# Performance work log

Hardware: AMD Instinct MI355X
Metric: run time of the kernel (lower is better)

## Reference

```python
import jax, jax.numpy as jnp
import numpy as np


def _maxpool2(x):
    # 2x2 max pool, stride 2, valid padding (H, W even). x: [B,H,W,C]
    B, H, W, C = x.shape
    return x.reshape(B, H // 2, 2, W // 2, 2, C).max(axis=(2, 4))


def setup_inputs() -> dict:
    key = jax.random.key(0)
    ks = jax.random.split(key, 9)
    B, H, W, C = 8, 64, 64, 512
    cfg, ch = C // 8, C // 2
    std = 0.02
    return {
        "x": jax.random.normal(ks[0], (B, H, W, C), jnp.float32),
        "theta_w": jax.random.normal(ks[1], (C, cfg), jnp.float32) * std,
        "theta_b": jnp.zeros((cfg,), jnp.float32),
        "phi_w": jax.random.normal(ks[2], (C, cfg), jnp.float32) * std,
        "phi_b": jnp.zeros((cfg,), jnp.float32),
        "g_w": jax.random.normal(ks[3], (C, ch), jnp.float32) * std,
        "g_b": jnp.zeros((ch,), jnp.float32),
        "o3_w": jax.random.normal(ks[4], (ch, C), jnp.float32) * std,
        "o3_b": jnp.zeros((C,), jnp.float32),
        # original initializes gamma to 0; use 0.1 so the attention branch contributes
        "gamma": jnp.full((1,), 0.1, jnp.float32),
    }


def reference(x, theta_w, theta_b, phi_w, phi_b, g_w, g_b, o3_w, o3_b, gamma):
    B, H, W, C = x.shape
    cfg = theta_w.shape[1]
    ch = g_w.shape[1]
    hw = H * W
    hwd = (H // 2) * (W // 2)

    theta = jnp.einsum("bhwc,cf->bhwf", x, theta_w) + theta_b          # [B,H,W,cfg]
    phi = _maxpool2(jnp.einsum("bhwc,cf->bhwf", x, phi_w) + phi_b)     # [B,H/2,W/2,cfg]
    g = _maxpool2(jnp.einsum("bhwc,cg->bhwg", x, g_w) + g_b)           # [B,H/2,W/2,ch]

    theta_f = theta.reshape(B, hw, cfg)
    phi_f = phi.reshape(B, hwd, cfg)
    g_f = g.reshape(B, hwd, ch)

    # s[b,i,j] = phi[b,i] . theta[b,j]; softmax over j (last axis, Keras default)
    s = jnp.einsum("bif,bjf->bij", phi_f, theta_f)                     # [B,hwd,hw]
    beta = jax.nn.softmax(s, axis=-1)
    # o = matmul(beta, g, transpose_a=True): o[b,j,c] = sum_i beta[b,i,j] g[b,i,c]
    o = jnp.einsum("bij,bic->bjc", beta, g_f)                          # [B,hw,ch]
    o = o.reshape(B, H, W, ch)
    o = jnp.einsum("bhwg,gc->bhwc", o, o3_w) + o3_b                    # [B,H,W,C]
    return gamma * o + x
```

## Files before the change

kernel.cpp:

```cpp
#include <hip/hip_runtime.h>
#include <cstdint>

typedef short short8 __attribute__((ext_vector_type(8)));
typedef float floatx4 __attribute__((ext_vector_type(4)));

__device__ __forceinline__ unsigned short f2bf(float f) {
    unsigned int u = __builtin_bit_cast(unsigned int, f);
    u += 0x7FFFu + ((u >> 16) & 1u);
    return (unsigned short)(u >> 16);
}
__device__ __forceinline__ float bf2f(unsigned short h) {
    unsigned int u = ((unsigned int)h) << 16;
    return __builtin_bit_cast(float, u);
}

__device__ __forceinline__ void async_copy16(const void* g, void* lds) {
    __builtin_amdgcn_global_load_lds(
        (const __attribute__((address_space(1))) void*)g,
        (__attribute__((address_space(3))) void*)lds, 16, 0, 0);
}

__device__ __forceinline__ int swz(int row, int koff) {
    return koff ^ (((row >> 2) & 3) << 4);
}

template<bool AFP32, int EPI>
__global__ __launch_bounds__(256) void mfma_gemm(
    const void* __restrict__ Avoid, const unsigned short* __restrict__ B,
    void* __restrict__ Cout, const float* __restrict__ bias,
    const float* __restrict__ gamma, const float* __restrict__ resid,
    int lda, int ldb, int ldc, int K)
{
    __shared__ unsigned short As[4096];
    __shared__ unsigned short Bs[4096];

    const int tid = threadIdx.x;
    const int wv = tid >> 6, ln = tid & 63;
    const int r16 = ln & 15, q8 = ln >> 4;
    const int wm = (wv >> 1) * 64, wn = (wv & 1) * 64;
    const int m0 = blockIdx.x * 128, n0 = blockIdx.y * 128;

    floatx4 acc[4][4] = {};

    for (int k0 = 0; k0 < K; k0 += 32) {
        if (AFP32) {
            const float* Af = (const float*)Avoid;
            #pragma unroll
            for (int p = 0; p < 4; ++p) {
                int u = p * 256 + tid;
                int row = u >> 3, c4 = u & 7;
                float4 v = *(const float4*)(Af + (size_t)(m0 + row) * lda + k0 + c4 * 4);
                ushort4 h;
                h.x = f2bf(v.x); h.y = f2bf(v.y); h.z = f2bf(v.z); h.w = f2bf(v.w);
                *(ushort4*)&As[row * 32 + c4 * 4] = h;
            }
            #pragma unroll
            for (int q = 0; q < 2; ++q) {
                int chunk = wv * 2 + q;
                int e = (chunk << 9) + ln * 8;
                int row = e >> 5, col = e & 31;
                async_copy16(B + (size_t)(n0 + row) * ldb + (k0 + col), &Bs[chunk << 9]);
            }
        } else {
            const unsigned short* Ag = (const unsigned short*)Avoid;
            #pragma unroll
            for (int q = 0; q < 2; ++q) {
                int chunk = wv * 2 + q;
                int e = (chunk << 9) + ln * 8;
                int row = e >> 5, col = e & 31;
                async_copy16(Ag + (size_t)(m0 + row) * lda + (k0 + col), &As[chunk << 9]);
                async_copy16(B + (size_t)(n0 + row) * ldb + (k0 + col), &Bs[chunk << 9]);
            }
        }
        __syncthreads();

        short8 af[4], bff[4];
        #pragma unroll
        for (int i = 0; i < 4; ++i) {
            af[i]  = *(const short8*)&As[(wm + i * 16 + r16) * 32 + q8 * 8];
            bff[i] = *(const short8*)&Bs[(wn + i * 16 + r16) * 32 + q8 * 8];
        }
        #pragma unroll
        for (int mi = 0; mi < 4; ++mi)
            #pragma unroll
            for (int ni = 0; ni < 4; ++ni)
                acc[mi][ni] = __builtin_amdgcn_mfma_f32_16x16x32_bf16(
                    af[mi], bff[ni], acc[mi][ni], 0, 0, 0);
        __syncthreads();
    }

    if (EPI == 2) {
        float* C = (float*)Cout;
        const float gm = gamma[0];
        #pragma unroll
        for (int ni = 0; ni < 4; ++ni) {
            const int n = n0 + wn + ni * 16 + r16;
            const float bs = bias[n];
            #pragma unroll
            for (int mi = 0; mi < 4; ++mi)
                #pragma unroll
                for (int r = 0; r < 4; ++r) {
                    int m = m0 + wm + mi * 16 + q8 * 4 + r;
                    C[(size_t)m * ldc + n] = gm * (acc[mi][ni][r] + bs) + resid[(size_t)m * ldc + n];
                }
        }
    } else {
        unsigned short* C = (unsigned short*)Cout;
        #pragma unroll
        for (int ni = 0; ni < 4; ++ni) {
            const int n = n0 + wn + ni * 16 + r16;
            const float bs = bias[n];
            #pragma unroll
            for (int mi = 0; mi < 4; ++mi)
                #pragma unroll
                for (int r = 0; r < 4; ++r) {
                    int m = m0 + wm + mi * 16 + q8 * 4 + r;
                    C[(size_t)m * ldc + n] = f2bf(acc[mi][ni][r] + bs);
                }
        }
    }
}

__global__ __launch_bounds__(256) void phase1_l_kernel(
    const unsigned short* __restrict__ tpgF,
    const unsigned short* __restrict__ phiP,
    float* __restrict__ lbuf)
{
    __shared__ unsigned short th_s[8192];
    __shared__ unsigned short ph_s[4096];
    const int tid = threadIdx.x, wv = tid >> 6, ln = tid & 63;
    const int r16 = ln & 15, q8 = ln >> 4, lsub = ln >> 3, l8 = ln & 7;
    const int jsp = blockIdx.x, i0 = blockIdx.y * 64, b = blockIdx.z;

    #pragma unroll
    for (int q = 0; q < 2; ++q) {
        int chunk = wv * 2 + q, row = chunk * 8 + lsub;
        int so = swz(row, l8 * 8);
        async_copy16(phiP + (size_t)(b * 1024 + i0 + row) * 64 + so, &ph_s[chunk * 512]);
    }

    float colsum[4] = {0.f, 0.f, 0.f, 0.f};
    for (int jc = 0; jc < 8; ++jc) {
        const int j0 = jsp * 1024 + jc * 128;
        __syncthreads();
        #pragma unroll
        for (int q = 0; q < 4; ++q) {
            int chunk = wv * 4 + q, row = chunk * 8 + lsub;
            int so = swz(row, l8 * 8);
            async_copy16(tpgF + (size_t)(b * 4096 + j0 + row) * 384 + so, &th_s[chunk * 512]);
        }
        __syncthreads();

        floatx4 sacc[2][4] = {};
        #pragma unroll
        for (int ks = 0; ks < 2; ++ks) {
            short8 af[2], bf[4];
            #pragma unroll
            for (int mi = 0; mi < 2; ++mi)
                af[mi] = *(const short8*)&th_s[(wv * 32 + mi * 16 + r16) * 64 + swz(r16, ks * 32 + q8 * 8)];
            #pragma unroll
            for (int ni = 0; ni < 4; ++ni)
                bf[ni] = *(const short8*)&ph_s[(ni * 16 + r16) * 64 + swz(r16, ks * 32 + q8 * 8)];
            #pragma unroll
            for (int mi = 0; mi < 2; ++mi)
                #pragma unroll
                for (int ni = 0; ni < 4; ++ni)
                    sacc[mi][ni] = __builtin_amdgcn_mfma_f32_16x16x32_bf16(
                        af[mi], bf[ni], sacc[mi][ni], 0, 0, 0);
        }
        #pragma unroll
        for (int mi = 0; mi < 2; ++mi)
            #pragma unroll
            for (int ni = 0; ni < 4; ++ni)
                #pragma unroll
                for (int r = 0; r < 4; ++r)
                    colsum[ni] += __expf(sacc[mi][ni][r] - 20.f);
    }
    #pragma unroll
    for (int ni = 0; ni < 4; ++ni) {
        float s = colsum[ni];
        s += __shfl_xor(s, 16);
        s += __shfl_xor(s, 32);
        if (q8 == 0) atomicAdd(&lbuf[b * 1024 + i0 + ni * 16 + r16], s);
    }
}

__global__ __launch_bounds__(512) void attn_fused_kernel(
    const unsigned short* __restrict__ tpgF,
    const unsigned short* __restrict__ phiP,
    const unsigned short* __restrict__ gPT,
    unsigned short* __restrict__ o_)
{
    __shared__ unsigned short es0[8192];
    __shared__ unsigned short es1[8192];
    __shared__ unsigned short ph_s[4][4096];
    __shared__ unsigned short gs[2][16384];

    const int tid = threadIdx.x, wv = tid >> 6, ln = tid & 63;
    const int r16 = ln & 15, q8 = ln >> 4, lsub = ln >> 3, l8 = ln & 7;
    const int j0 = blockIdx.x * 128, b = blockIdx.y;
    const int jh = wv >> 2, it = wv & 3;

    #pragma unroll
    for (int q = 0; q < 2; ++q) {
        int chunk = wv * 2 + q, row = chunk * 8 + lsub;
        async_copy16(tpgF + (size_t)(b * 4096 + j0 + row) * 384 + swz(row, l8 * 8),
                     &es1[chunk * 512]);
    }
    {
        int prow = wv * 8 + lsub;
        async_copy16(phiP + (size_t)(b * 1024 + prow) * 64 + swz(prow, l8 * 8),
                     &ph_s[0][wv * 512]);
        #pragma unroll
        for (int q = 0; q < 4; ++q) {
            int chunk = wv * 4 + q, c = chunk * 8 + lsub;
            async_copy16(gPT + (size_t)(b * 256 + c) * 1024 + swz(c, l8 * 8),
                         &gs[0][chunk * 512]);
        }
        async_copy16(phiP + (size_t)(b * 1024 + 64 + prow) * 64 + swz(prow, l8 * 8),
                     &ph_s[1][wv * 512]);
    }
    asm volatile("s_waitcnt vmcnt(5)" ::: "memory");
    __builtin_amdgcn_sched_barrier(0);
    __builtin_amdgcn_s_barrier();
    __builtin_amdgcn_sched_barrier(0);

    short8 thf[4][2];
    #pragma unroll
    for (int mi = 0; mi < 4; ++mi)
        #pragma unroll
        for (int ks = 0; ks < 2; ++ks)
            thf[mi][ks] = *(const short8*)&es1[(jh * 64 + mi * 16 + r16) * 64
                                               + swz(r16, ks * 32 + q8 * 8)];

    {
        floatx4 sacc[4] = {};
        #pragma unroll
        for (int ks = 0; ks < 2; ++ks) {
            short8 pf = *(const short8*)&ph_s[0][(it * 16 + r16) * 64
                                                 + swz(r16, ks * 32 + q8 * 8)];
            #pragma unroll
            for (int mi = 0; mi < 4; ++mi)
                sacc[mi] = __builtin_amdgcn_mfma_f32_16x16x32_bf16(
                    thf[mi][ks], pf, sacc[mi], 0, 0, 0);
        }
        #pragma unroll
        for (int mi = 0; mi < 4; ++mi)
            #pragma unroll
            for (int r = 0; r < 4; ++r) {
                int j = jh * 64 + mi * 16 + q8 * 4 + r;
                es0[j * 64 + (((it ^ q8) << 4) | r16)] = f2bf(__expf(sacc[mi][r] - 20.f));
            }
    }
    asm volatile("s_waitcnt vmcnt(0) lgkmcnt(0)" ::: "memory");
    __builtin_amdgcn_sched_barrier(0);
    __builtin_amdgcn_s_barrier();
    __builtin_amdgcn_sched_barrier(0);

    floatx4 acc[4][4] = {};

    for (int t = 0; t < 16; ++t) {
        const int buf = t & 1, nbuf = buf ^ 1;
        unsigned short* esr = buf ? es1 : es0;
        unsigned short* esw = buf ? es0 : es1;
        const unsigned short* gsr = gs[buf];
        unsigned short* gsw = gs[nbuf];

        if (t < 15) {
            #pragma unroll
            for (int q = 0; q < 4; ++q) {
                int chunk = wv * 4 + q, c = chunk * 8 + lsub;
                async_copy16(gPT + (size_t)(b * 256 + c) * 1024 + (t + 1) * 64 + swz(c, l8 * 8),
                             &gsw[chunk * 512]);
            }
        }
        if (t < 14) {
            int prow = wv * 8 + lsub;
            async_copy16(phiP + (size_t)(b * 1024 + (t + 2) * 64 + prow) * 64 + swz(prow, l8 * 8),
                         &ph_s[(t + 2) & 3][wv * 512]);
        }

        if (t < 15) {
            const unsigned short* php = ph_s[(t + 1) & 3];
            floatx4 sacc[4] = {};
            #pragma unroll
            for (int ks = 0; ks < 2; ++ks) {
                short8 pf = *(const short8*)&php[(it * 16 + r16) * 64
                                                 + swz(r16, ks * 32 + q8 * 8)];
                #pragma unroll
                for (int mi = 0; mi < 4; ++mi)
                    sacc[mi] = __builtin_amdgcn_mfma_f32_16x16x32_bf16(
                        thf[mi][ks], pf, sacc[mi], 0, 0, 0);
            }
            #pragma unroll
            for (int mi = 0; mi < 4; ++mi)
                #pragma unroll
                for (int r = 0; r < 4; ++r) {
                    int j = jh * 64 + mi * 16 + q8 * 4 + r;
                    esw[j * 64 + (((it ^ q8) << 4) | r16)] = f2bf(__expf(sacc[mi][r] - 20.f));
                }
        }

        #pragma unroll
        for (int ks = 0; ks < 2; ++ks) {
            short8 ef[4], gf[4];
            #pragma unroll
            for (int mi = 0; mi < 4; ++mi)
                ef[mi] = *(const short8*)&esr[(jh * 64 + mi * 16 + r16) * 64
                                              + swz(r16, ks * 32 + q8 * 8)];
            #pragma unroll
            for (int ni = 0; ni < 4; ++ni)
                gf[ni] = *(const short8*)&gsr[(it * 64 + ni * 16 + r16) * 64
                                              + swz(r16, ks * 32 + q8 * 8)];
            __builtin_amdgcn_s_setprio(1);
            #pragma unroll
            for (int mi = 0; mi < 4; ++mi)
                #pragma unroll
                for (int ni = 0; ni < 4; ++ni)
                    acc[mi][ni] = __builtin_amdgcn_mfma_f32_16x16x32_bf16(
                        ef[mi], gf[ni], acc[mi][ni], 0, 0, 0);
            __builtin_amdgcn_s_setprio(0);
        }

        if (t < 15) {
            asm volatile("s_waitcnt vmcnt(0) lgkmcnt(0)" ::: "memory");
            __builtin_amdgcn_sched_barrier(0);
            __builtin_amdgcn_s_barrier();
            __builtin_amdgcn_sched_barrier(0);
        }
    }

    #pragma unroll
    for (int mi = 0; mi < 4; ++mi)
        #pragma unroll
        for (int ni = 0; ni < 4; ++ni)
            #pragma unroll
            for (int r = 0; r < 4; ++r) {
                int j = j0 + jh * 64 + mi * 16 + q8 * 4 + r;
                int c = it * 64 + ni * 16 + r16;
                o_[((size_t)b * 4096 + j) * 256 + c] = f2bf(acc[mi][ni][r]);
            }
}

__global__ __launch_bounds__(256) void prep_w_kernel(
    const float* __restrict__ theta_w, const float* __restrict__ phi_w,
    const float* __restrict__ g_w, const float* __restrict__ o3_w,
    const float* __restrict__ theta_b, const float* __restrict__ phi_b,
    const float* __restrict__ g_b,
    unsigned short* __restrict__ tpgwT, unsigned short* __restrict__ o3wT,
    float* __restrict__ biasTPG, float* __restrict__ lbuf)
{
    int t = blockIdx.x * 256 + threadIdx.x;
    if (t < 196608) {
        int n = t >> 9, k = t & 511;
        float v = (n < 64) ? theta_w[k * 64 + n]
                : (n < 128) ? phi_w[k * 64 + (n - 64)]
                : g_w[k * 256 + (n - 128)];
        tpgwT[t] = f2bf(v);
    } else if (t < 327680) {
        int e = t - 196608; int n = e >> 8, k = e & 255;
        o3wT[e] = f2bf(o3_w[k * 512 + n]);
    } else if (t < 328064) {
        int j = t - 327680;
        biasTPG[j] = (j < 64) ? theta_b[j] : (j < 128) ? phi_b[j - 64] : g_b[j - 128];
    } else if (t < 336256) {
        lbuf[t - 328064] = 0.f;
    }
}

__global__ __launch_bounds__(256) void maxpool_phi_kernel(
    const unsigned short* __restrict__ tpgF, unsigned short* __restrict__ phiP)
{
    int t = blockIdx.x * 256 + threadIdx.x;
    int f = t & 63, i = (t >> 6) & 1023, b = t >> 16;
    int ph = i >> 5, pw = i & 31;
    size_t base = ((size_t)(b * 64 + 2 * ph) * 64 + 2 * pw) * 384 + 64 + f;
    float v0 = bf2f(tpgF[base]),         v1 = bf2f(tpgF[base + 384]);
    float v2 = bf2f(tpgF[base + 24576]), v3 = bf2f(tpgF[base + 24576 + 384]);
    phiP[t] = f2bf(fmaxf(fmaxf(v0, v1), fmaxf(v2, v3)));
}

__global__ __launch_bounds__(256) void maxpoolT_g_kernel(
    const unsigned short* __restrict__ tpgF, const float* __restrict__ lbuf,
    unsigned short* __restrict__ gPT)
{
    __shared__ unsigned short tile[16][256];
    __shared__ float rls[16];
    int b = blockIdx.y, i0 = blockIdx.x * 16, c = threadIdx.x;
    if (c < 16) rls[c] = 1.0f / lbuf[b * 1024 + i0 + c];
    __syncthreads();
    #pragma unroll
    for (int il = 0; il < 16; ++il) {
        int i = i0 + il, ph = i >> 5, pw = i & 31;
        size_t base = ((size_t)(b * 64 + 2 * ph) * 64 + 2 * pw) * 384 + 128 + c;
        float v0 = bf2f(tpgF[base]),         v1 = bf2f(tpgF[base + 384]);
        float v2 = bf2f(tpgF[base + 24576]), v3 = bf2f(tpgF[base + 24576 + 384]);
        tile[il][c] = f2bf(fmaxf(fmaxf(v0, v1), fmaxf(v2, v3)) * rls[il]);
    }
    __syncthreads();
    unsigned short* dst = gPT + ((size_t)(b * 256 + c) * 1024 + i0);
    short8 v0, v1;
    #pragma unroll
    for (int il = 0; il < 8; ++il) { v0[il] = (short)tile[il][c]; v1[il] = (short)tile[il + 8][c]; }
    *(short8*)dst = v0;
    *(short8*)(dst + 8) = v1;
}

extern "C" void kernel_launch(void* const* d_in, const int* in_sizes, int n_in,
                              void* d_out, int out_size, void* d_ws, size_t ws_size,
                              hipStream_t stream)
{
    const float* x       = (const float*)d_in[0];
    const float* theta_w = (const float*)d_in[1];
    const float* theta_b = (const float*)d_in[2];
    const float* phi_w   = (const float*)d_in[3];
    const float* phi_b   = (const float*)d_in[4];
    const float* g_w     = (const float*)d_in[5];
    const float* g_b     = (const float*)d_in[6];
    const float* o3_w    = (const float*)d_in[7];
    const float* o3_b    = (const float*)d_in[8];
    const float* gamma   = (const float*)d_in[9];

    char* ws = (char*)d_ws;
    unsigned short* tpgwT  = (unsigned short*)(ws);
    unsigned short* o3wT   = (unsigned short*)(ws + 393216);
    float* biasTPG         = (float*)(ws + 655360);
    float* lbuf            = (float*)(ws + 656896);
    unsigned short* tpgF   = (unsigned short*)(ws + (1u << 20));
    unsigned short* phiP   = (unsigned short*)(ws + (1u << 20) + 25165824);
    unsigned short* gPT    = (unsigned short*)(ws + (1u << 20) + 26214400);
    unsigned short* o_     = (unsigned short*)(ws + (1u << 20) + 30408704);

    prep_w_kernel<<<1314, 256, 0, stream>>>(theta_w, phi_w, g_w, o3_w,
                                            theta_b, phi_b, g_b,
                                            tpgwT, o3wT, biasTPG, lbuf);
    mfma_gemm<true, 1><<<dim3(256, 3), 256, 0, stream>>>(
        x, tpgwT, tpgF, biasTPG, nullptr, nullptr, 512, 512, 384, 512);
    maxpool_phi_kernel<<<2048, 256, 0, stream>>>(tpgF, phiP);
    phase1_l_kernel<<<dim3(4, 16, 8), 256, 0, stream>>>(tpgF, phiP, lbuf);
    maxpoolT_g_kernel<<<dim3(64, 8), 256, 0, stream>>>(tpgF, lbuf, gPT);
    attn_fused_kernel<<<dim3(32, 8), 512, 0, stream>>>(tpgF, phiP, gPT, o_);
    mfma_gemm<false, 2><<<dim3(256, 4), 256, 0, stream>>>(
        o_, o3wT, d_out, o3_b, gamma, x, 256, 256, 512, 256);
}
```

Baseline: 227.0 us.

## Split attention kernel into smaller 64x128 tiles and swap GEMM grid axes

The fused attention kernel now uses 256-thread blocks, each covering 64 query rows and half of the 256 output channels. The grid grows from 256 to 1024 blocks, LDS per block shrinks, and launch bounds allow two blocks per CU. This is meant to improve occupancy and spread work across more CUs, at the cost of computing the exp(score) tiles twice, once per channel half. The GEMM grids are also transposed so that blocks sharing the same A rows launch next to each other, which should improve L2 reuse of A.

```diff
diff --git a/kernel.cpp b/kernel.cpp
--- a/kernel.cpp
+++ b/kernel.cpp
@@ -38,7 +38,7 @@
     const int wv = tid >> 6, ln = tid & 63;
     const int r16 = ln & 15, q8 = ln >> 4;
     const int wm = (wv >> 1) * 64, wn = (wv & 1) * 64;
-    const int m0 = blockIdx.x * 128, n0 = blockIdx.y * 128;
+    const int m0 = blockIdx.y * 128, n0 = blockIdx.x * 128;
 
     floatx4 acc[4][4] = {};
 
@@ -185,21 +185,21 @@
     }
 }
 
-__global__ __launch_bounds__(512) void attn_fused_kernel(
+__global__ __launch_bounds__(256, 2) void attn_fused_kernel(
     const unsigned short* __restrict__ tpgF,
     const unsigned short* __restrict__ phiP,
     const unsigned short* __restrict__ gPT,
     unsigned short* __restrict__ o_)
 {
-    __shared__ unsigned short es0[8192];
-    __shared__ unsigned short es1[8192];
-    __shared__ unsigned short ph_s[4][4096];
-    __shared__ unsigned short gs[2][16384];
+    __shared__ unsigned short es0[4096];
+    __shared__ unsigned short es1[4096];
+    __shared__ unsigned short ph_s[3][4096];
+    __shared__ unsigned short gs[2][8192];
 
     const int tid = threadIdx.x, wv = tid >> 6, ln = tid & 63;
     const int r16 = ln & 15, q8 = ln >> 4, lsub = ln >> 3, l8 = ln & 7;
-    const int j0 = blockIdx.x * 128, b = blockIdx.y;
-    const int jh = wv >> 2, it = wv & 3;
+    const int j0 = blockIdx.x * 64, c0 = blockIdx.y * 128, b = blockIdx.z;
+    const int jh = wv >> 1, icq = wv & 1;
 
     #pragma unroll
     for (int q = 0; q < 2; ++q) {
@@ -207,49 +207,52 @@
         async_copy16(tpgF + (size_t)(b * 4096 + j0 + row) * 384 + swz(row, l8 * 8),
                      &es1[chunk * 512]);
     }
-    {
-        int prow = wv * 8 + lsub;
-        async_copy16(phiP + (size_t)(b * 1024 + prow) * 64 + swz(prow, l8 * 8),
-                     &ph_s[0][wv * 512]);
-        #pragma unroll
-        for (int q = 0; q < 4; ++q) {
-            int chunk = wv * 4 + q, c = chunk * 8 + lsub;
-            async_copy16(gPT + (size_t)(b * 256 + c) * 1024 + swz(c, l8 * 8),
-                         &gs[0][chunk * 512]);
-        }
-        async_copy16(phiP + (size_t)(b * 1024 + 64 + prow) * 64 + swz(prow, l8 * 8),
-                     &ph_s[1][wv * 512]);
-    }
-    asm volatile("s_waitcnt vmcnt(5)" ::: "memory");
+    #pragma unroll
+    for (int q = 0; q < 2; ++q) {
+        int chunk = wv * 2 + q, row = chunk * 8 + lsub;
+        async_copy16(phiP + (size_t)(b * 1024 + row) * 64 + swz(row, l8 * 8),
+                     &ph_s[0][chunk * 512]);
+    }
+    #pragma unroll
+    for (int q = 0; q < 4; ++q) {
+        int chunk = wv * 4 + q, crow = chunk * 8 + lsub;
+        async_copy16(gPT + (size_t)(b * 256 + c0 + crow) * 1024 + swz(crow, l8 * 8),
+                     &gs[0][chunk * 512]);
+    }
+    #pragma unroll
+    for (int q = 0; q < 2; ++q) {
+        int chunk = wv * 2 + q, row = chunk * 8 + lsub;
+        async_copy16(phiP + (size_t)(b * 1024 + 64 + row) * 64 + swz(row, l8 * 8),
+                     &ph_s[1][chunk * 512]);
+    }
+    asm volatile("s_waitcnt vmcnt(6)" ::: "memory");
     __builtin_amdgcn_sched_barrier(0);
     __builtin_amdgcn_s_barrier();
     __builtin_amdgcn_sched_barrier(0);
 
-    short8 thf[4][2];
-    #pragma unroll
-    for (int mi = 0; mi < 4; ++mi)
-        #pragma unroll
-        for (int ks = 0; ks < 2; ++ks)
-            thf[mi][ks] = *(const short8*)&es1[(jh * 64 + mi * 16 + r16) * 64
-                                               + swz(r16, ks * 32 + q8 * 8)];
+    short8 thf[2];
+    #pragma unroll
+    for (int ks = 0; ks < 2; ++ks)
+        thf[ks] = *(const short8*)&es1[(wv * 16 + r16) * 64 + swz(r16, ks * 32 + q8 * 8)];
 
     {
         floatx4 sacc[4] = {};
         #pragma unroll
         for (int ks = 0; ks < 2; ++ks) {
-            short8 pf = *(const short8*)&ph_s[0][(it * 16 + r16) * 64
-                                                 + swz(r16, ks * 32 + q8 * 8)];
-            #pragma unroll
-            for (int mi = 0; mi < 4; ++mi)
-                sacc[mi] = __builtin_amdgcn_mfma_f32_16x16x32_bf16(
-                    thf[mi][ks], pf, sacc[mi], 0, 0, 0);
-        }
-        #pragma unroll
-        for (int mi = 0; mi < 4; ++mi)
+            #pragma unroll
+            for (int ni = 0; ni < 4; ++ni) {
+                short8 pf = *(const short8*)&ph_s[0][(ni * 16 + r16) * 64
+                                                     + swz(r16, ks * 32 + q8 * 8)];
+                sacc[ni] = __builtin_amdgcn_mfma_f32_16x16x32_bf16(
+                    thf[ks], pf, sacc[ni], 0, 0, 0);
+            }
+        }
+        #pragma unroll
+        for (int ni = 0; ni < 4; ++ni)
             #pragma unroll
             for (int r = 0; r < 4; ++r) {
-                int j = jh * 64 + mi * 16 + q8 * 4 + r;
-                es0[j * 64 + (((it ^ q8) << 4) | r16)] = f2bf(__expf(sacc[mi][r] - 20.f));
+                int j = wv * 16 + q8 * 4 + r;
+                es0[j * 64 + (((ni ^ q8) << 4) | r16)] = f2bf(__expf(sacc[ni][r] - 20.f));
             }
     }
     asm volatile("s_waitcnt vmcnt(0) lgkmcnt(0)" ::: "memory");
@@ -257,64 +260,71 @@
     __builtin_amdgcn_s_barrier();
     __builtin_amdgcn_sched_barrier(0);
 
-    floatx4 acc[4][4] = {};
+    floatx4 acc[2][4] = {};
 
     for (int t = 0; t < 16; ++t) {
-        const int buf = t & 1, nbuf = buf ^ 1;
+        const int buf = t & 1;
         unsigned short* esr = buf ? es1 : es0;
         unsigned short* esw = buf ? es0 : es1;
         const unsigned short* gsr = gs[buf];
-        unsigned short* gsw = gs[nbuf];
+        unsigned short* gsw = gs[buf ^ 1];
 
         if (t < 15) {
             #pragma unroll
             for (int q = 0; q < 4; ++q) {
-                int chunk = wv * 4 + q, c = chunk * 8 + lsub;
-                async_copy16(gPT + (size_t)(b * 256 + c) * 1024 + (t + 1) * 64 + swz(c, l8 * 8),
+                int chunk = wv * 4 + q, crow = chunk * 8 + lsub;
+                async_copy16(gPT + (size_t)(b * 256 + c0 + crow) * 1024 + (t + 1) * 64
+                                 + swz(crow, l8 * 8),
                              &gsw[chunk * 512]);
             }
         }
         if (t < 14) {
-            int prow = wv * 8 + lsub;
-            async_copy16(phiP + (size_t)(b * 1024 + (t + 2) * 64 + prow) * 64 + swz(prow, l8 * 8),
-                         &ph_s[(t + 2) & 3][wv * 512]);
+            unsigned short* php = ph_s[(t + 2) % 3];
+            #pragma unroll
+            for (int q = 0; q < 2; ++q) {
+                int chunk = wv * 2 + q, row = chunk * 8 + lsub;
+                async_copy16(phiP + (size_t)(b * 1024 + (t + 2) * 64 + row) * 64
+                                  + swz(row, l8 * 8),
+                             &php[chunk * 512]);
+            }
         }
 
         if (t < 15) {
-            const unsigned short* php = ph_s[(t + 1) & 3];
+            const unsigned short* php = ph_s[(t + 1) % 3];
             floatx4 sacc[4] = {};
             #pragma unroll
             for (int ks = 0; ks < 2; ++ks) {
-                short8 pf = *(const short8*)&php[(it * 16 + r16) * 64
-                                                 + swz(r16, ks * 32 + q8 * 8)];
-                #pragma unroll
-                for (int mi = 0; mi < 4; ++mi)
-                    sacc[mi] = __builtin_amdgcn_mfma_f32_16x16x32_bf16(
-                        thf[mi][ks], pf, sacc[mi], 0, 0, 0);
-            }
-            #pragma unroll
-            for (int mi = 0; mi < 4; ++mi)
+                #pragma unroll
+                for (int ni = 0; ni < 4; ++ni) {
+                    short8 pf = *(const short8*)&php[(ni * 16 + r16) * 64
+                                                     + swz(r16, ks * 32 + q8 * 8)];
+                    sacc[ni] = __builtin_amdgcn_mfma_f32_16x16x32_bf16(
+                        thf[ks], pf, sacc[ni], 0, 0, 0);
+                }
+            }
+            #pragma unroll
+            for (int ni = 0; ni < 4; ++ni)
                 #pragma unroll
                 for (int r = 0; r < 4; ++r) {
-                    int j = jh * 64 + mi * 16 + q8 * 4 + r;
-                    esw[j * 64 + (((it ^ q8) << 4) | r16)] = f2bf(__expf(sacc[mi][r] - 20.f));
+                    int j = wv * 16 + q8 * 4 + r;
+                    esw[j * 64 + (((ni ^ q8) << 4) | r16)] = f2bf(__expf(sacc[ni][r] - 20.f));
                 }
         }
 
         #pragma unroll
         for (int ks = 0; ks < 2; ++ks) {
-            short8 ef[4], gf[4];
-            #pragma unroll
-            for (int mi = 0; mi < 4; ++mi)
-                ef[mi] = *(const short8*)&esr[(jh * 64 + mi * 16 + r16) * 64
+            short8 ef[2], gf[4];
+            #pragma unroll
+            for (int mi = 0; mi < 2; ++mi)
+                ef[mi] = *(const short8*)&esr[(jh * 32 + mi * 16 + r16) * 64
                                               + swz(r16, ks * 32 + q8 * 8)];
             #pragma unroll
             for (int ni = 0; ni < 4; ++ni)
-                gf[ni] = *(const short8*)&gsr[(it * 64 + ni * 16 + r16) * 64
+                gf[ni] = *(const short8*)&gsr[(icq * 64 + ni * 16 + r16) * 64
                                               + swz(r16, ks * 32 + q8 * 8)];
             __builtin_amdgcn_s_setprio(1);
             #pragma unroll
-            for (int mi = 0; mi < 4; ++mi)
+            for (int mi = 0; mi < 2; ++mi)
                 #pragma unroll
                 for (int ni = 0; ni < 4; ++ni)
                     acc[mi][ni] = __builtin_amdgcn_mfma_f32_16x16x32_bf16(
@@ -331,13 +341,13 @@
     }
 
     #pragma unroll
-    for (int mi = 0; mi < 4; ++mi)
+    for (int mi = 0; mi < 2; ++mi)
         #pragma unroll
         for (int ni = 0; ni < 4; ++ni)
             #pragma unroll
             for (int r = 0; r < 4; ++r) {
-                int j = j0 + jh * 64 + mi * 16 + q8 * 4 + r;
-                int c = it * 64 + ni * 16 + r16;
+                int j = j0 + jh * 32 + mi * 16 + q8 * 4 + r;
+                int c = c0 + icq * 64 + ni * 16 + r16;
                 o_[((size_t)b * 4096 + j) * 256 + c] = f2bf(acc[mi][ni][r]);
             }
 }
@@ -434,12 +444,12 @@
     prep_w_kernel<<<1314, 256, 0, stream>>>(theta_w, phi_w, g_w, o3_w,
                                             theta_b, phi_b, g_b,
                                             tpgwT, o3wT, biasTPG, lbuf);
-    mfma_gemm<true, 1><<<dim3(256, 3), 256, 0, stream>>>(
+    mfma_gemm<true, 1><<<dim3(3, 256), 256, 0, stream>>>(
         x, tpgwT, tpgF, biasTPG, nullptr, nullptr, 512, 512, 384, 512);
     maxpool_phi_kernel<<<2048, 256, 0, stream>>>(tpgF, phiP);
     phase1_l_kernel<<<dim3(4, 16, 8), 256, 0, stream>>>(tpgF, phiP, lbuf);
     maxpoolT_g_kernel<<<dim3(64, 8), 256, 0, stream>>>(tpgF, lbuf, gPT);
-    attn_fused_kernel<<<dim3(32, 8), 512, 0, stream>>>(tpgF, phiP, gPT, o_);
-    mfma_gemm<false, 2><<<dim3(256, 4), 256, 0, stream>>>(
+    attn_fused_kernel<<<dim3(64, 2, 8), 256, 0, stream>>>(tpgF, phiP, gPT, o_);
+    mfma_gemm<false, 2><<<dim3(4, 256), 256, 0, stream>>>(
         o_, o3wT, d_out, o3_b, gamma, x, 256, 256, 512, 256);
 }
```

Result: slower. 253.3 us (+11.6%).
